# Kernel optimization log

Measured on AMD Instinct MI355X. Metric: run time of the kernel, lower is better.

The kernel has to match this reference:

```python
import jax, jax.numpy as jnp
import numpy as np

N_Q = 9      # qubits -> state dim 512
N_L = 10     # circuit layers
DIM = 2 ** N_Q
B = 16384    # batch
N_CLS = 10


def _apply_1q(psi, U, q):
    # psi: [B, 2,...,2] (N_Q qubit axes); U: [2,2] complex
    psi = jnp.moveaxis(psi, q + 1, 1)
    shp = psi.shape
    psi = jnp.einsum('ij,bjk->bik', U, psi.reshape(shp[0], 2, -1)).reshape(shp)
    return jnp.moveaxis(psi, 1, q + 1)


def _apply_2q(psi, U, q0, q1):
    # U: [4,4] complex acting on (q0, q1)
    psi = jnp.moveaxis(psi, (q0 + 1, q1 + 1), (1, 2))
    shp = psi.shape
    psi = jnp.einsum('ij,bjk->bik', U, psi.reshape(shp[0], 4, -1)).reshape(shp)
    return jnp.moveaxis(psi, (1, 2), (q0 + 1, q1 + 1))


def _rot_mat(phi, theta, omega):
    # PennyLane Rot = RZ(omega) RY(theta) RZ(phi)
    c, s = jnp.cos(theta / 2), jnp.sin(theta / 2)
    a, b = (phi + omega) / 2, (phi - omega) / 2
    return jnp.stack([
        jnp.stack([jnp.exp(-1j * a) * c, -jnp.exp(1j * b) * s]),
        jnp.stack([jnp.exp(-1j * b) * s, jnp.exp(1j * a) * c]),
    ]).astype(jnp.complex64)


def _crx_mat(t):
    c, s = jnp.cos(t / 2), jnp.sin(t / 2)
    rx = jnp.stack([jnp.stack([c + 0j, -1j * s]),
                    jnp.stack([-1j * s, c + 0j])]).astype(jnp.complex64)
    return jnp.eye(4, dtype=jnp.complex64).at[2:, 2:].set(rx)


def _layer(psi, rot_n, crx_n):
    for i in range(N_Q):
        psi = _apply_1q(psi, _rot_mat(rot_n[i, 0], rot_n[i, 1], rot_n[i, 2]), i)
    for i in range(N_Q):
        psi = _apply_2q(psi, _crx_mat(crx_n[i, 0]), i, (i + 1) % N_Q)
    return psi


def _circuit(x, rot, crx):
    # AmplitudeEmbedding(normalize=True)
    psi = (x / jnp.linalg.norm(x, axis=1, keepdims=True)).astype(jnp.complex64)
    psi = psi.reshape((x.shape[0],) + (2,) * N_Q)
    for n in range(N_L):
        psi = _layer(psi, rot[n], crx[n])
    probs = psi.real ** 2 + psi.imag ** 2
    # <Z_q> = P(bit_q = 0) - P(bit_q = 1)
    zs = []
    for q in range(N_Q):
        axes = tuple(a for a in range(1, N_Q + 1) if a != q + 1)
        p = probs.sum(axis=axes)  # [B, 2]
        zs.append(p[:, 0] - p[:, 1])
    return jnp.stack(zs, axis=1)  # [B, N_Q]


def setup_inputs() -> dict:
    key = jax.random.key(0)
    k0, k1, k2, k3, k4 = jax.random.split(key, 5)
    x = jax.random.normal(k0, (B, DIM), jnp.float32)
    rot = jax.random.normal(k1, (N_L, N_Q, 3), jnp.float32)
    crx = jax.random.normal(k2, (N_L, N_Q, 1), jnp.float32)
    fc_w = jax.random.normal(k3, (N_CLS, N_Q), jnp.float32) * 0.3
    fc_b = jax.random.normal(k4, (N_CLS,), jnp.float32) * 0.1
    return {"x": x, "rot": rot, "crx": crx, "fc_w": fc_w, "fc_b": fc_b}


def reference(x, rot, crx, fc_w, fc_b):
    z = _circuit(x, rot, crx)          # [B, 9]
    logits = z @ fc_w.T + fc_b         # [B, 10]
    return jax.nn.log_softmax(logits, axis=1)
```

## Files before the change

kernel.cpp:

```cpp
#include <hip/hip_runtime.h>
#include <hip/hip_bf16.h>
#include <math.h>

#define NQ 9
#define NL 10
#define DIM 512
#define NCLS 10
#define B_TOT 16384

#define A_OFF   ((size_t)0)
#define BT_OFF  ((size_t)16 << 20)
#define ZP_OFF  ((size_t)32 << 20)
#define WS_NEED (((size_t)96) << 20)

__device__ __forceinline__ float shx(float v, int m) { return __shfl_xor(v, m, 64); }

__device__ __forceinline__ int looks_bf16(const void* p, int count) {
  const unsigned short* u = (const unsigned short*)p;
  int n = count < 64 ? count : 64;
  int good = 0;
  for (int i = 0; i < n; ++i) {
    unsigned short v = u[i];
    int e = (v >> 7) & 0xFF;
    good += (e >= 100 && e <= 140) || ((v & 0x7FFF) == 0);
  }
  return good * 8 >= n * 7;
}

__device__ __forceinline__ float ld(const void* p, int i, int isbf) {
  if (isbf) return __uint_as_float(((unsigned)((const unsigned short*)p)[i]) << 16);
  return ((const float*)p)[i];
}

template<int M>
__device__ __forceinline__ void rot_x(float (&sr)[8], float (&si)[8], const float* u) {
  float4 uA = *(const float4*)u;
  float4 uB = *(const float4*)(u + 4);
  bool hi = (threadIdx.x & M) != 0;
  float ar = hi ? uB.z : uA.x, ai = hi ? uB.w : uA.y;
  float br = hi ? uB.x : uA.z, bi = hi ? uB.y : uA.w;
#pragma unroll
  for (int r = 0; r < 8; ++r) {
    float pr = shx(sr[r], M), pi = shx(si[r], M);
    float nr = ar * sr[r] - ai * si[r] + br * pr - bi * pi;
    float ni = ar * si[r] + ai * sr[r] + br * pi + bi * pr;
    sr[r] = nr; si[r] = ni;
  }
}
template<int S>
__device__ __forceinline__ void rot_r(float (&sr)[8], float (&si)[8], const float* u) {
  float4 uA = *(const float4*)u;
  float4 uB = *(const float4*)(u + 4);
#pragma unroll
  for (int r0 = 0; r0 < 8; ++r0) {
    if (r0 & S) continue;
    int r1 = r0 + S;
    float a0r = sr[r0], a0i = si[r0], a1r = sr[r1], a1i = si[r1];
    sr[r0] = uA.x * a0r - uA.y * a0i + uA.z * a1r - uA.w * a1i;
    si[r0] = uA.x * a0i + uA.y * a0r + uA.z * a1i + uA.w * a1r;
    sr[r1] = uB.x * a0r - uB.y * a0i + uB.z * a1r - uB.w * a1i;
    si[r1] = uB.x * a0i + uB.y * a0r + uB.z * a1i + uB.w * a1r;
  }
}
template<int MC, int MT>
__device__ __forceinline__ void crx_ll(float (&sr)[8], float (&si)[8], const float* cs) {
  bool ctrl = (threadIdx.x & MC) != 0;
  float c = ctrl ? cs[0] : 1.0f;
  float s = ctrl ? cs[1] : 0.0f;
#pragma unroll
  for (int r = 0; r < 8; ++r) {
    float pr = shx(sr[r], MT), pi = shx(si[r], MT);
    float nr = c * sr[r] + s * pi;
    float ni = c * si[r] - s * pr;
    sr[r] = nr; si[r] = ni;
  }
}
template<int MC, int ST>
__device__ __forceinline__ void crx_lr(float (&sr)[8], float (&si)[8], const float* cs) {
  bool ctrl = (threadIdx.x & MC) != 0;
  float c = ctrl ? cs[0] : 1.0f;
  float s = ctrl ? cs[1] : 0.0f;
#pragma unroll
  for (int r0 = 0; r0 < 8; ++r0) {
    if (r0 & ST) continue;
    int r1 = r0 + ST;
    float a0r = sr[r0], a0i = si[r0], a1r = sr[r1], a1i = si[r1];
    sr[r0] = c * a0r + s * a1i;  si[r0] = c * a0i - s * a1r;
    sr[r1] = c * a1r + s * a0i;  si[r1] = c * a1i - s * a0r;
  }
}
template<int PC, int ST>
__device__ __forceinline__ void crx_rr(float (&sr)[8], float (&si)[8], const float* cs) {
  float c = cs[0], s = cs[1];
#pragma unroll
  for (int r0 = 0; r0 < 8; ++r0) {
    if (r0 & ST) continue;
    if (!((r0 >> PC) & 1)) continue;
    int r1 = r0 + ST;
    float a0r = sr[r0], a0i = si[r0], a1r = sr[r1], a1i = si[r1];
    sr[r0] = c * a0r + s * a1i;  si[r0] = c * a0i - s * a1r;
    sr[r1] = c * a1r + s * a0i;  si[r1] = c * a1i - s * a0r;
  }
}
template<int PC, int MT>
__device__ __forceinline__ void crx_rl(float (&sr)[8], float (&si)[8], const float* cs) {
  float c = cs[0], s = cs[1];
#pragma unroll
  for (int r = 0; r < 8; ++r) {
    if (!((r >> PC) & 1)) continue;
    float pr = shx(sr[r], MT), pi = shx(si[r], MT);
    float nr = c * sr[r] + s * pi;
    float ni = c * si[r] - s * pr;
    sr[r] = nr; si[r] = ni;
  }
}

__device__ __forceinline__ void build_gates(const void* rot, const void* crx,
                                            float* gU, float* gCS) {
  int tid = threadIdx.x;
  __shared__ int gflags[2];
  if (tid == 0) {
    gflags[0] = looks_bf16(rot, NL * NQ * 3);
    gflags[1] = looks_bf16(crx, NL * NQ);
  }
  __syncthreads();
  if (tid < NL * NQ) {
    int frot = gflags[0], fcrx = gflags[1];
    float phi = ld(rot, tid * 3 + 0, frot);
    float th  = ld(rot, tid * 3 + 1, frot);
    float om  = ld(rot, tid * 3 + 2, frot);
    float c = cosf(0.5f * th), s = sinf(0.5f * th);
    float a = 0.5f * (phi + om), b = 0.5f * (phi - om);
    float ca = cosf(a), sa = sinf(a), cb = cosf(b), sb = sinf(b);
    float* u = gU + tid * 8;
    u[0] =  ca * c; u[1] = -sa * c;
    u[2] = -cb * s; u[3] = -sb * s;
    u[4] =  cb * s; u[5] = -sb * s;
    u[6] =  ca * c; u[7] =  sa * c;
    float t2 = 0.5f * ld(crx, tid, fcrx);
    gCS[tid * 2 + 0] = cosf(t2);
    gCS[tid * 2 + 1] = sinf(t2);
  }
  __syncthreads();
}

__device__ __forceinline__ void run_circuit(float (&sr)[8], float (&si)[8],
                                            const float* gU, const float* gCS) {
#pragma unroll 1
  for (int n = 0; n < NL; ++n) {
    const float* U  = gU  + n * NQ * 8;
    const float* CS = gCS + n * NQ * 2;
    rot_x<32>(sr, si, U + 0 * 8);
    rot_x<16>(sr, si, U + 1 * 8);
    rot_x< 8>(sr, si, U + 2 * 8);
    rot_x< 4>(sr, si, U + 3 * 8);
    rot_x< 2>(sr, si, U + 4 * 8);
    rot_x< 1>(sr, si, U + 5 * 8);
    rot_r< 4>(sr, si, U + 6 * 8);
    rot_r< 2>(sr, si, U + 7 * 8);
    rot_r< 1>(sr, si, U + 8 * 8);
    crx_ll<32, 16>(sr, si, CS + 0 * 2);
    crx_ll<16,  8>(sr, si, CS + 1 * 2);
    crx_ll< 8,  4>(sr, si, CS + 2 * 2);
    crx_ll< 4,  2>(sr, si, CS + 3 * 2);
    crx_ll< 2,  1>(sr, si, CS + 4 * 2);
    crx_lr< 1,  4>(sr, si, CS + 5 * 2);
    crx_rr< 2,  2>(sr, si, CS + 6 * 2);
    crx_rr< 1,  1>(sr, si, CS + 7 * 2);
    crx_rl< 0, 32>(sr, si, CS + 8 * 2);
  }
}

template<int M>
__device__ __forceinline__ void rot_lane2(float (&sr)[2], float (&si)[2], const float* u) {
  float4 uA = *(const float4*)u;
  float4 uB = *(const float4*)(u + 4);
  bool hi = (threadIdx.x & M) != 0;
  float ar = hi ? uB.z : uA.x, ai = hi ? uB.w : uA.y;
  float br = hi ? uB.x : uA.z, bi = hi ? uB.y : uA.w;
#pragma unroll
  for (int r = 0; r < 2; ++r) {
    float pr = shx(sr[r], M), pi = shx(si[r], M);
    float nr = ar * sr[r] - ai * si[r] + br * pr - bi * pi;
    float ni = ar * si[r] + ai * sr[r] + br * pi + bi * pr;
    sr[r] = nr; si[r] = ni;
  }
}
__device__ __forceinline__ void rot_reg2(float (&sr)[2], float (&si)[2], const float* u) {
  float4 uA = *(const float4*)u;
  float4 uB = *(const float4*)(u + 4);
  float a0r = sr[0], a0i = si[0], a1r = sr[1], a1i = si[1];
  sr[0] = uA.x * a0r - uA.y * a0i + uA.z * a1r - uA.w * a1i;
  si[0] = uA.x * a0i + uA.y * a0r + uA.z * a1i + uA.w * a1r;
  sr[1] = uB.x * a0r - uB.y * a0i + uB.z * a1r - uB.w * a1i;
  si[1] = uB.x * a0i + uB.y * a0r + uB.z * a1i + uB.w * a1r;
}
__device__ __forceinline__ void crx_lane2(float (&sr)[2], float (&si)[2],
                                          float c, float s, int MT) {
#pragma unroll
  for (int r = 0; r < 2; ++r) {
    float pr = shx(sr[r], MT), pi = shx(si[r], MT);
    float nr = c * sr[r] + s * pi;
    float ni = c * si[r] - s * pr;
    sr[r] = nr; si[r] = ni;
  }
}
__device__ __forceinline__ void crx_reg2(float (&sr)[2], float (&si)[2], float c, float s) {
  float a0r = sr[0], a0i = si[0], a1r = sr[1], a1i = si[1];
  sr[0] = c * a0r + s * a1i;  si[0] = c * a0i - s * a1r;
  sr[1] = c * a1r + s * a0i;  si[1] = c * a1i - s * a0r;
}

__global__ __launch_bounds__(256) void prep_kernel(const void* __restrict__ x,
                                                   const void* __restrict__ rot,
                                                   const void* __restrict__ crx,
                                                   __hip_bfloat16* __restrict__ A,
                                                   __hip_bfloat16* __restrict__ BT) {
  int tid = threadIdx.x;
  if (blockIdx.x < DIM) {
    __shared__ __align__(16) float gU[NL * NQ * 8];
    __shared__ __align__(16) float gCS[NL * NQ * 2];
    __shared__ float sRe[DIM], sIm[DIM];
    build_gates(rot, crx, gU, gCS);
    int lane = tid & 63, wv = tid >> 6;
    int idx0 = wv * 128 + lane * 2;
    int k = blockIdx.x;
    float sr[2], si[2];
    sr[0] = (idx0 == k) ? 1.f : 0.f;
    sr[1] = (idx0 + 1 == k) ? 1.f : 0.f;
    si[0] = si[1] = 0.f;
#pragma unroll 1
    for (int n = 0; n < NL; ++n) {
      const float* U   = gU  + n * NQ * 8;
      const float* CS  = gCS + n * NQ * 2;
      const float* CSp = gCS + (n - 1) * NQ * 2;
      __syncthreads();
      sRe[idx0] = sr[0]; sIm[idx0] = si[0];
      sRe[idx0 + 1] = sr[1]; sIm[idx0 + 1] = si[1];
      __syncthreads();
      {
        const float* U0 = U; const float* U1 = U + 8;
        int a = wv >> 1, b = wv & 1;
        float mr[4], mi[4];
#pragma unroll
        for (int w2 = 0; w2 < 4; ++w2) {
          int a2 = w2 >> 1, b2 = w2 & 1;
          float u0r = U0[(a * 2 + a2) * 2], u0i = U0[(a * 2 + a2) * 2 + 1];
          float u1r = U1[(b * 2 + b2) * 2], u1i = U1[(b * 2 + b2) * 2 + 1];
          mr[w2] = u0r * u1r - u0i * u1i;
          mi[w2] = u0r * u1i + u0i * u1r;
        }
        float x0r[4], x0i[4], v1r[4], v1i[4];
#pragma unroll
        for (int w2 = 0; w2 < 4; ++w2) {
          x0r[w2] = sRe[w2 * 128 + lane * 2 + 0];
          x0i[w2] = sIm[w2 * 128 + lane * 2 + 0];
          v1r[w2] = sRe[w2 * 128 + lane * 2 + 1];
          v1i[w2] = sIm[w2 * 128 + lane * 2 + 1];
        }
        float x1r[4], x1i[4];
        if (n > 0) {
          float cp = CSp[16], sp = CSp[17];
#pragma unroll
          for (int w2 = 0; w2 < 4; ++w2) {
            x1r[w2] = cp * v1r[w2] + sp * v1i[w2 ^ 2];
            x1i[w2] = cp * v1i[w2] - sp * v1r[w2 ^ 2];
          }
        } else {
#pragma unroll
          for (int w2 = 0; w2 < 4; ++w2) { x1r[w2] = v1r[w2]; x1i[w2] = v1i[w2]; }
        }
        float nr0 = 0.f, ni0 = 0.f, nr1 = 0.f, ni1 = 0.f;
#pragma unroll
        for (int w2 = 0; w2 < 4; ++w2) {
          nr0 += mr[w2] * x0r[w2] - mi[w2] * x0i[w2];
          ni0 += mr[w2] * x0i[w2] + mi[w2] * x0r[w2];
          nr1 += mr[w2] * x1r[w2] - mi[w2] * x1i[w2];
          ni1 += mr[w2] * x1i[w2] + mi[w2] * x1r[w2];
        }
        sr[0] = nr0; si[0] = ni0; sr[1] = nr1; si[1] = ni1;
      }
      rot_lane2<32>(sr, si, U + 2 * 8);
      rot_lane2<16>(sr, si, U + 3 * 8);
      rot_lane2< 8>(sr, si, U + 4 * 8);
      rot_lane2< 4>(sr, si, U + 5 * 8);
      rot_lane2< 2>(sr, si, U + 6 * 8);
      rot_lane2< 1>(sr, si, U + 7 * 8);
      rot_reg2(sr, si, U + 8 * 8);
      __syncthreads();
      sRe[idx0] = sr[0]; sIm[idx0] = si[0];
      sRe[idx0 + 1] = sr[1]; sIm[idx0 + 1] = si[1];
      __syncthreads();
      {
        float c = (wv & 2) ? CS[0] : 1.f, s = (wv & 2) ? CS[1] : 0.f;
        int p0 = (wv ^ 1) * 128 + lane * 2;
#pragma unroll
        for (int r = 0; r < 2; ++r) {
          float pr = sRe[p0 + r], pi = sIm[p0 + r];
          float nr = c * sr[r] + s * pi;
          float ni = c * si[r] - s * pr;
          sr[r] = nr; si[r] = ni;
        }
      }
      { float c = (wv & 1) ? CS[2] : 1.f, s = (wv & 1) ? CS[3] : 0.f;
        crx_lane2(sr, si, c, s, 32); }
      { bool ct = (lane & 32); crx_lane2(sr, si, ct ? CS[4] : 1.f, ct ? CS[5] : 0.f, 16); }
      { bool ct = (lane & 16); crx_lane2(sr, si, ct ? CS[6] : 1.f, ct ? CS[7] : 0.f, 8); }
      { bool ct = (lane &  8); crx_lane2(sr, si, ct ? CS[8] : 1.f, ct ? CS[9] : 0.f, 4); }
      { bool ct = (lane &  4); crx_lane2(sr, si, ct ? CS[10] : 1.f, ct ? CS[11] : 0.f, 2); }
      { bool ct = (lane &  2); crx_lane2(sr, si, ct ? CS[12] : 1.f, ct ? CS[13] : 0.f, 1); }
      { bool ct = (lane & 1); crx_reg2(sr, si, ct ? CS[14] : 1.f, ct ? CS[15] : 0.f); }
    }
    __syncthreads();
    sRe[idx0] = sr[0]; sIm[idx0] = si[0];
    sRe[idx0 + 1] = sr[1]; sIm[idx0 + 1] = si[1];
    __syncthreads();
    {
      const float* CS9 = gCS + (NL - 1) * NQ * 2;
      float c = CS9[16], s = CS9[17];
      int p1 = (wv ^ 2) * 128 + lane * 2 + 1;
      float pr = sRe[p1], pi = sIm[p1];
      float nr = c * sr[1] + s * pi;
      float ni = c * si[1] - s * pr;
      sr[1] = nr; si[1] = ni;
    }
#pragma unroll
    for (int r = 0; r < 2; ++r) {
      int j = idx0 + r;
      BT[(size_t)j * DIM + k]         = __float2bfloat16(sr[r]);
      BT[(size_t)(DIM + j) * DIM + k] = __float2bfloat16(si[r]);
    }
  } else {
    __shared__ int fx;
    if (tid == 0) fx = looks_bf16(x, B_TOT * DIM);
    __syncthreads();
    size_t i0 = ((size_t)(blockIdx.x - DIM) * 256 + tid) * 8;
    if (fx) {
      *(uint4*)(A + i0) = *(const uint4*)((const unsigned short*)x + i0);
    } else {
      const float4* src = (const float4*)((const float*)x + i0);
      float4 a = src[0], b = src[1];
      __hip_bfloat16 o[8];
      o[0] = __float2bfloat16(a.x); o[1] = __float2bfloat16(a.y);
      o[2] = __float2bfloat16(a.z); o[3] = __float2bfloat16(a.w);
      o[4] = __float2bfloat16(b.x); o[5] = __float2bfloat16(b.y);
      o[6] = __float2bfloat16(b.z); o[7] = __float2bfloat16(b.w);
      *(uint4*)(A + i0) = *(uint4*)o;
    }
  }
}

using frag8 = __attribute__((ext_vector_type(8))) short;
using frag4 = __attribute__((ext_vector_type(4))) float;

typedef __attribute__((address_space(1))) const unsigned int GU32;
typedef __attribute__((address_space(3))) unsigned int LU32;
__device__ __forceinline__ void async16(const void* g, void* l) {
  __builtin_amdgcn_global_load_lds((GU32*)g, (LU32*)l, 16, 0, 0);
}

#define PPITCH 136
#define PANEL (128 * 32)

__global__ __launch_bounds__(256) void gemm_z_kernel(const unsigned short* __restrict__ A,
                                                     const unsigned short* __restrict__ BT,
                                                     float* __restrict__ Zp) {
  __shared__ __align__(16) unsigned short lsm[128 * PPITCH + 16 * PPITCH];
  unsigned short* lA0 = lsm;
  unsigned short* lA1 = lsm + PANEL;
  unsigned short* lB0 = lsm + 2 * PANEL;
  unsigned short* lB1 = lsm + 3 * PANEL;
  unsigned short* pA  = lsm;
  unsigned short* STm = lsm + 128 * PPITCH;
  int bid = blockIdx.x;
  int xcd = bid & 7;
  int slot = bid >> 3;
  int n0 = (slot & 7) * 128;
  int m0 = (xcd * 16 + (slot >> 3)) * 128;
  int tid = threadIdx.x;
  int wv = tid >> 6, lane = tid & 63;
  int wm = wv >> 1, wn = wv & 1;
  int row = lane & 15, quad = lane >> 4;
  for (int i = tid; i < 16 * 128; i += 256) {
    int q = i >> 7, k2 = i & 127;
    int j = (n0 + k2) & 511;
    float sg = (q < 9) ? (((j >> (8 - q)) & 1) ? -1.f : 1.f) : (q == 9 ? 1.f : 0.f);
    __hip_bfloat16 h = __float2bfloat16(sg);
    STm[q * PPITCH + k2] = *(unsigned short*)&h;
  }
  int srow = wv * 32 + (lane >> 2);
  int scol = (lane & 3) * 8;
  const unsigned short* gA = A + (size_t)(m0 + srow) * 512 + scol;
  const unsigned short* gB = BT + (size_t)(n0 + srow) * 512 + scol;
  frag4 acc[4][4] = {};
#pragma unroll 1
  for (int k0 = 0; k0 < 512; k0 += 64) {
    __syncthreads();
    async16(gA + k0,                 &lA0[(wv * 32) * 32]);
    async16(gA + k0 + 16 * 512,      &lA0[(wv * 32 + 16) * 32]);
    async16(gA + k0 + 32,            &lA1[(wv * 32) * 32]);
    async16(gA + k0 + 32 + 16 * 512, &lA1[(wv * 32 + 16) * 32]);
    async16(gB + k0,                 &lB0[(wv * 32) * 32]);
    async16(gB + k0 + 16 * 512,      &lB0[(wv * 32 + 16) * 32]);
    async16(gB + k0 + 32,            &lB1[(wv * 32) * 32]);
    async16(gB + k0 + 32 + 16 * 512, &lB1[(wv * 32 + 16) * 32]);
    __syncthreads();
    {
      frag8 af[4], bf[4];
#pragma unroll
      for (int i = 0; i < 4; ++i) {
        af[i] = *(const frag8*)(&lA0[(wm * 64 + i * 16 + row) * 32 + quad * 8]);
        bf[i] = *(const frag8*)(&lB0[(wn * 64 + i * 16 + row) * 32 + quad * 8]);
      }
#pragma unroll
      for (int mi = 0; mi < 4; ++mi)
#pragma unroll
        for (int ni = 0; ni < 4; ++ni)
          acc[mi][ni] = __builtin_amdgcn_mfma_f32_16x16x32_bf16(af[mi], bf[ni],
                                                                acc[mi][ni], 0, 0, 0);
    }
    {
      frag8 af[4], bf[4];
#pragma unroll
      for (int i = 0; i < 4; ++i) {
        af[i] = *(const frag8*)(&lA1[(wm * 64 + i * 16 + row) * 32 + quad * 8]);
        bf[i] = *(const frag8*)(&lB1[(wn * 64 + i * 16 + row) * 32 + quad * 8]);
      }
#pragma unroll
      for (int mi = 0; mi < 4; ++mi)
#pragma unroll
        for (int ni = 0; ni < 4; ++ni)
          acc[mi][ni] = __builtin_amdgcn_mfma_f32_16x16x32_bf16(af[mi], bf[ni],
                                                                acc[mi][ni], 0, 0, 0);
    }
  }
  __syncthreads();
#pragma unroll
  for (int mi = 0; mi < 4; ++mi)
#pragma unroll
    for (int ni = 0; ni < 4; ++ni)
#pragma unroll
      for (int rg = 0; rg < 4; ++rg) {
        float v = acc[mi][ni][rg];
        float p = v * v;
        int mrow = wm * 64 + mi * 16 + quad * 4 + rg;
        int k2 = wn * 64 + ni * 16 + row;
        __hip_bfloat16 h = __float2bfloat16(p);
        pA[mrow * PPITCH + k2] = *(unsigned short*)&h;
      }
  __syncthreads();
  frag8 b2[4];
#pragma unroll
  for (int kk = 0; kk < 4; ++kk)
    b2[kk] = *(const frag8*)(&STm[row * PPITCH + kk * 32 + quad * 8]);
  frag4 zacc2[2] = {};
#pragma unroll
  for (int t = 0; t < 2; ++t) {
    int mt = wv + t * 4;
#pragma unroll
    for (int kk = 0; kk < 4; ++kk) {
      frag8 a2 = *(const frag8*)(&pA[(mt * 16 + row) * PPITCH + kk * 32 + quad * 8]);
      zacc2[t] = __builtin_amdgcn_mfma_f32_16x16x32_bf16(a2, b2[kk], zacc2[t], 0, 0, 0);
    }
  }
  int panel = n0 >> 7;
  if (row < 10) {
#pragma unroll
    for (int t = 0; t < 2; ++t) {
      int mt = wv + t * 4;
#pragma unroll
      for (int rg = 0; rg < 4; ++rg) {
        int mrow = m0 + mt * 16 + quad * 4 + rg;
        Zp[(size_t)panel * (B_TOT * 10) + (size_t)mrow * 10 + row] = zacc2[t][rg];
      }
    }
  }
}

__global__ __launch_bounds__(256) void zred_kernel(const float* __restrict__ Zp,
                                                   const void* __restrict__ fcw,
                                                   const void* __restrict__ fcb,
                                                   float* __restrict__ out) {
  __shared__ int flags[2];
  __shared__ float sW[NCLS * NQ];
  __shared__ float sB[NCLS];
  int tid = threadIdx.x;
  if (tid == 0) {
    flags[0] = looks_bf16(fcw, NCLS * NQ);
    flags[1] = looks_bf16(fcb, NCLS);
  }
  __syncthreads();
  if (tid < NCLS * NQ) sW[tid] = ld(fcw, tid, flags[0]);
  if (tid < NCLS)      sB[tid] = ld(fcb, tid, flags[1]);
  __syncthreads();
  int row = blockIdx.x * 256 + tid;
  float z[10];
#pragma unroll
  for (int q = 0; q < 10; ++q) z[q] = 0.f;
#pragma unroll
  for (int pnl = 0; pnl < 8; ++pnl) {
    const float* p = Zp + (size_t)pnl * (B_TOT * 10) + (size_t)row * 10;
#pragma unroll
    for (int q = 0; q < 10; ++q) z[q] += p[q];
  }
  float invP = 1.0f / z[9];
#pragma unroll
  for (int q = 0; q < NQ; ++q) z[q] *= invP;
  float lg[NCLS], mx = -1e30f;
#pragma unroll
  for (int k = 0; k < NCLS; ++k) {
    float t = sB[k];
#pragma unroll
    for (int q = 0; q < NQ; ++q) t += z[q] * sW[k * NQ + q];
    lg[k] = t; mx = fmaxf(mx, t);
  }
  float se = 0.f;
#pragma unroll
  for (int k = 0; k < NCLS; ++k) se += expf(lg[k] - mx);
  float lse = mx + logf(se);
#pragma unroll
  for (int k = 0; k < NCLS; ++k) out[(size_t)row * NCLS + k] = lg[k] - lse;
}

__global__ __launch_bounds__(256) void qnn_kernel(
    const void* __restrict__ x, const void* __restrict__ rot,
    const void* __restrict__ crx, const void* __restrict__ fcw,
    const void* __restrict__ fcb, float* __restrict__ out) {
  __shared__ __align__(16) float gU[NL * NQ * 8];
  __shared__ __align__(16) float gCS[NL * NQ * 2];
  __shared__ int flags[3];
  int tid = threadIdx.x;
  if (tid == 0) {
    flags[0] = looks_bf16(x, B_TOT * DIM);
    flags[1] = looks_bf16(fcw, NCLS * NQ);
    flags[2] = looks_bf16(fcb, NCLS);
  }
  build_gates(rot, crx, gU, gCS);
  __syncthreads();
  int wid = (blockIdx.x * blockDim.x + tid) >> 6;
  int lane = tid & 63;
  float sr[8], si[8];
  if (flags[0]) {
    const uint4 u = *(const uint4*)((const unsigned short*)x + (size_t)wid * DIM + lane * 8);
    sr[0] = __uint_as_float(u.x << 16); sr[1] = __uint_as_float(u.x & 0xffff0000u);
    sr[2] = __uint_as_float(u.y << 16); sr[3] = __uint_as_float(u.y & 0xffff0000u);
    sr[4] = __uint_as_float(u.z << 16); sr[5] = __uint_as_float(u.z & 0xffff0000u);
    sr[6] = __uint_as_float(u.w << 16); sr[7] = __uint_as_float(u.w & 0xffff0000u);
  } else {
    const float4* xf = (const float4*)((const float*)x + (size_t)wid * DIM) + lane * 2;
    float4 a = xf[0], b = xf[1];
    sr[0] = a.x; sr[1] = a.y; sr[2] = a.z; sr[3] = a.w;
    sr[4] = b.x; sr[5] = b.y; sr[6] = b.z; sr[7] = b.w;
  }
  float nrm = 0.f;
#pragma unroll
  for (int r = 0; r < 8; ++r) { nrm += sr[r] * sr[r]; si[r] = 0.f; }
#pragma unroll
  for (int m = 1; m < 64; m <<= 1) nrm += shx(nrm, m);
  float inv = rsqrtf(nrm);
  inv = inv * (1.5f - 0.5f * nrm * inv * inv);
#pragma unroll
  for (int r = 0; r < 8; ++r) sr[r] *= inv;
  run_circuit(sr, si, gU, gCS);
  float p[8], P = 0.f;
#pragma unroll
  for (int r = 0; r < 8; ++r) { p[r] = sr[r] * sr[r] + si[r] * si[r]; P += p[r]; }
  float z[NQ];
#pragma unroll
  for (int q = 0; q < 6; ++q) z[q] = (lane & (32 >> q)) ? -P : P;
  z[6] = z[7] = z[8] = 0.f;
#pragma unroll
  for (int r = 0; r < 8; ++r) {
    z[6] += (r & 4) ? -p[r] : p[r];
    z[7] += (r & 2) ? -p[r] : p[r];
    z[8] += (r & 1) ? -p[r] : p[r];
  }
#pragma unroll
  for (int m = 1; m < 64; m <<= 1) {
#pragma unroll
    for (int q = 0; q < NQ; ++q) z[q] += shx(z[q], m);
  }
  int ffw = flags[1], ffb = flags[2];
  float lg[NCLS], mx = -1e30f;
#pragma unroll
  for (int k = 0; k < NCLS; ++k) {
    float t = ld(fcb, k, ffb);
#pragma unroll
    for (int q = 0; q < NQ; ++q) t += z[q] * ld(fcw, k * NQ + q, ffw);
    lg[k] = t; mx = fmaxf(mx, t);
  }
  float se = 0.f;
#pragma unroll
  for (int k = 0; k < NCLS; ++k) se += expf(lg[k] - mx);
  float lse = mx + logf(se);
  if (lane < NCLS) out[(size_t)wid * NCLS + lane] = lg[lane] - lse;
}

extern "C" void kernel_launch(void* const* d_in, const int* in_sizes, int n_in,
                              void* d_out, int out_size, void* d_ws, size_t ws_size,
                              hipStream_t stream) {
  const void* x   = d_in[0];
  const void* rot = d_in[1];
  const void* crx = d_in[2];
  const void* fcw = d_in[3];
  const void* fcb = d_in[4];
  float* out = (float*)d_out;
  if (ws_size >= WS_NEED) {
    __hip_bfloat16* A  = (__hip_bfloat16*)((char*)d_ws + A_OFF);
    __hip_bfloat16* BT = (__hip_bfloat16*)((char*)d_ws + BT_OFF);
    float*          Zp = (float*)((char*)d_ws + ZP_OFF);
    prep_kernel<<<DIM + (B_TOT * DIM) / (256 * 8), 256, 0, stream>>>(x, rot, crx, A, BT);
    gemm_z_kernel<<<(B_TOT / 128) * (1024 / 128), 256, 0, stream>>>(
        (const unsigned short*)A, (const unsigned short*)BT, Zp);
    zred_kernel<<<B_TOT / 256, 256, 0, stream>>>(Zp, fcw, fcb, out);
  } else {
    qnn_kernel<<<(B_TOT * 64) / 256, 256, 0, stream>>>(x, rot, crx, fcw, fcb, out);
  }
}
```

Before: 143.2 us.

## Rewrite GEMM as 256x256 tiles with double-buffered async loads and swizzled LDS

```diff
diff --git a/kernel.cpp b/kernel.cpp
--- a/kernel.cpp
+++ b/kernel.cpp
@@ -359,125 +359,155 @@
   __builtin_amdgcn_global_load_lds((GU32*)g, (LU32*)l, 16, 0, 0);
 }
 
-#define PPITCH 136
-#define PANEL (128 * 32)
-
-__global__ __launch_bounds__(256) void gemm_z_kernel(const unsigned short* __restrict__ A,
-                                                     const unsigned short* __restrict__ BT,
-                                                     float* __restrict__ Zp) {
-  __shared__ __align__(16) unsigned short lsm[128 * PPITCH + 16 * PPITCH];
-  unsigned short* lA0 = lsm;
-  unsigned short* lA1 = lsm + PANEL;
-  unsigned short* lB0 = lsm + 2 * PANEL;
-  unsigned short* lB1 = lsm + 3 * PANEL;
-  unsigned short* pA  = lsm;
-  unsigned short* STm = lsm + 128 * PPITCH;
+#define VM(N) asm volatile("s_waitcnt vmcnt(" #N ")" ::: "memory")
+#define BARR  do { __builtin_amdgcn_sched_barrier(0); \
+                   __builtin_amdgcn_s_barrier(); \
+                   __builtin_amdgcn_sched_barrier(0); } while (0)
+
+#define STG_A(NB, T1, H) do { \
+  async16(gA + ((size_t)((H) * 128) * 512 + (T1) * 64),     dA + (NB) * 16384 + (H) * 8192); \
+  async16(gA + ((size_t)((H) * 128 + 8) * 512 + (T1) * 64), dA + (NB) * 16384 + (H) * 8192 + 512); \
+} while (0)
+#define STG_B(NB, T1, H) do { \
+  async16(gB + ((size_t)((H) * 128) * 512 + (T1) * 64),     dB + (NB) * 16384 + (H) * 8192); \
+  async16(gB + ((size_t)((H) * 128 + 8) * 512 + (T1) * 64), dB + (NB) * 16384 + (H) * 8192 + 512); \
+} while (0)
+
+#define PHASE(CURB, QM, QN, STG, VMC) do { \
+  frag8 paf[4][2], pbf[2][2]; \
+  _Pragma("unroll") \
+  for (int mi = 0; mi < 4; ++mi) { \
+    _Pragma("unroll") \
+    for (int kk = 0; kk < 2; ++kk) \
+      paf[mi][kk] = *(const frag8*)(lsm + (CURB) * 16384 + \
+        ((QM) * 128 + wm * 64 + mi * 16 + r15) * 64 + \
+        (((kk * 4 + quad) ^ (r15 & 7)) * 8)); \
+  } \
+  _Pragma("unroll") \
+  for (int ni = 0; ni < 2; ++ni) { \
+    _Pragma("unroll") \
+    for (int kk = 0; kk < 2; ++kk) \
+      pbf[ni][kk] = *(const frag8*)(lsm + 32768 + (CURB) * 16384 + \
+        ((QN) * 128 + wn * 32 + ni * 16 + r15) * 64 + \
+        (((kk * 4 + quad) ^ (r15 & 7)) * 8)); \
+  } \
+  STG; \
+  __builtin_amdgcn_s_setprio(1); \
+  _Pragma("unroll") \
+  for (int mi = 0; mi < 4; ++mi) { \
+    _Pragma("unroll") \
+    for (int ni = 0; ni < 2; ++ni) { \
+      acc[QM][mi][QN][ni] = __builtin_amdgcn_mfma_f32_16x16x32_bf16( \
+          paf[mi][0], pbf[ni][0], acc[QM][mi][QN][ni], 0, 0, 0); \
+      acc[QM][mi][QN][ni] = __builtin_amdgcn_mfma_f32_16x16x32_bf16( \
+          paf[mi][1], pbf[ni][1], acc[QM][mi][QN][ni], 0, 0, 0); \
+    } \
+  } \
+  __builtin_amdgcn_s_setprio(0); \
+  VMC; \
+} while (0)
+
+__global__ __launch_bounds__(512, 2) void gemm_z_kernel(const unsigned short* __restrict__ A,
+                                                        const unsigned short* __restrict__ BT,
+                                                        float* __restrict__ Zp) {
+  __shared__ __align__(16) unsigned short lsm[65536];
   int bid = blockIdx.x;
   int xcd = bid & 7;
-  int slot = bid >> 3;
-  int n0 = (slot & 7) * 128;
-  int m0 = (xcd * 16 + (slot >> 3)) * 128;
+  int ii = bid >> 3;
+  int m0 = (xcd * 8 + (ii >> 2)) * 256;
+  int n0 = (ii & 3) * 256;
   int tid = threadIdx.x;
   int wv = tid >> 6, lane = tid & 63;
-  int wm = wv >> 1, wn = wv & 1;
-  int row = lane & 15, quad = lane >> 4;
-  for (int i = tid; i < 16 * 128; i += 256) {
-    int q = i >> 7, k2 = i & 127;
-    int j = (n0 + k2) & 511;
-    float sg = (q < 9) ? (((j >> (8 - q)) & 1) ? -1.f : 1.f) : (q == 9 ? 1.f : 0.f);
-    __hip_bfloat16 h = __float2bfloat16(sg);
-    STm[q * PPITCH + k2] = *(unsigned short*)&h;
-  }
-  int srow = wv * 32 + (lane >> 2);
-  int scol = (lane & 3) * 8;
-  const unsigned short* gA = A + (size_t)(m0 + srow) * 512 + scol;
-  const unsigned short* gB = BT + (size_t)(n0 + srow) * 512 + scol;
-  frag4 acc[4][4] = {};
+  int wm = wv >> 2, wn = wv & 3;
+  int r15 = lane & 15, quad = lane >> 4;
+  int lr3 = lane >> 3;
+  int scol = ((lane & 7) ^ lr3) * 8;
+  const unsigned short* gA = A + (size_t)(m0 + wv * 16 + lr3) * 512 + scol;
+  const unsigned short* gB = BT + (size_t)(n0 + wv * 16 + lr3) * 512 + scol;
+  unsigned short* dA = lsm + wv * 16 * 64;
+  unsigned short* dB = lsm + 32768 + wv * 16 * 64;
+
+  frag4 acc[2][4][2][2] = {};
+
+  STG_A(0, 0, 0); STG_B(0, 0, 0); STG_A(0, 0, 1); STG_B(0, 0, 1);
+  VM(4);
+  BARR;
+
 #pragma unroll 1
-  for (int k0 = 0; k0 < 512; k0 += 64) {
-    __syncthreads();
-    async16(gA + k0,                 &lA0[(wv * 32) * 32]);
-    async16(gA + k0 + 16 * 512,      &lA0[(wv * 32 + 16) * 32]);
-    async16(gA + k0 + 32,            &lA1[(wv * 32) * 32]);
-    async16(gA + k0 + 32 + 16 * 512, &lA1[(wv * 32 + 16) * 32]);
-    async16(gB + k0,                 &lB0[(wv * 32) * 32]);
-    async16(gB + k0 + 16 * 512,      &lB0[(wv * 32 + 16) * 32]);
-    async16(gB + k0 + 32,            &lB1[(wv * 32) * 32]);
-    async16(gB + k0 + 32 + 16 * 512, &lB1[(wv * 32 + 16) * 32]);
-    __syncthreads();
-    {
-      frag8 af[4], bf[4];
-#pragma unroll
-      for (int i = 0; i < 4; ++i) {
-        af[i] = *(const frag8*)(&lA0[(wm * 64 + i * 16 + row) * 32 + quad * 8]);
-        bf[i] = *(const frag8*)(&lB0[(wn * 64 + i * 16 + row) * 32 + quad * 8]);
-      }
-#pragma unroll
-      for (int mi = 0; mi < 4; ++mi)
-#pragma unroll
-        for (int ni = 0; ni < 4; ++ni)
-          acc[mi][ni] = __builtin_amdgcn_mfma_f32_16x16x32_bf16(af[mi], bf[ni],
-                                                                acc[mi][ni], 0, 0, 0);
+  for (int t = 0; t < 7; ++t) {
+    const int cur = t & 1, nb = cur ^ 1;
+    PHASE(cur, 0, 0, STG_A(nb, t + 1, 0), VM(4)); BARR;
+    PHASE(cur, 1, 0, STG_B(nb, t + 1, 0), VM(4)); BARR;
+    PHASE(cur, 0, 1, STG_A(nb, t + 1, 1), ;);
+    PHASE(cur, 1, 1, STG_B(nb, t + 1, 1), VM(4)); BARR;
+  }
+  PHASE(1, 0, 0, ;, VM(2)); BARR;
+  PHASE(1, 1, 0, ;, VM(0)); BARR;
+  PHASE(1, 0, 1, ;, ;);
+  PHASE(1, 1, 1, ;, ;);
+  __syncthreads();
+
+#pragma unroll
+  for (int qm = 0; qm < 2; ++qm)
+#pragma unroll
+    for (int mi = 0; mi < 4; ++mi)
+#pragma unroll
+      for (int qn = 0; qn < 2; ++qn)
+#pragma unroll
+        for (int ni = 0; ni < 2; ++ni)
+#pragma unroll
+          for (int rg = 0; rg < 4; ++rg) {
+            float v = acc[qm][mi][qn][ni][rg];
+            float p = v * v;
+            int prow = qm * 128 + wm * 64 + mi * 16 + quad * 4 + rg;
+            int pcol = qn * 128 + wn * 32 + ni * 16 + r15;
+            int phys = (pcol >> 3) ^ (prow & 7);
+            __hip_bfloat16 h = __float2bfloat16(p);
+            lsm[prow * 256 + phys * 8 + (pcol & 7)] = *(unsigned short*)&h;
+          }
+  __syncthreads();
+
+  frag8 b2[8];
+#pragma unroll
+  for (int kk = 0; kk < 8; ++kk) {
+    union { frag8 f; unsigned short u[8]; } bb;
+#pragma unroll
+    for (int e = 0; e < 8; ++e) {
+      int j = (n0 + kk * 32 + quad * 8 + e) & 511;
+      unsigned short us;
+      if (r15 < 9)      us = ((((unsigned)j) >> ((8 - r15) & 31)) & 1) ? 0xBF80 : 0x3F80;
+      else if (r15 == 9) us = 0x3F80;
+      else               us = 0;
+      bb.u[e] = us;
     }
-    {
-      frag8 af[4], bf[4];
-#pragma unroll
-      for (int i = 0; i < 4; ++i) {
-        af[i] = *(const frag8*)(&lA1[(wm * 64 + i * 16 + row) * 32 + quad * 8]);
-        bf[i] = *(const frag8*)(&lB1[(wn * 64 + i * 16 + row) * 32 + quad * 8]);
-      }
-#pragma unroll
-      for (int mi = 0; mi < 4; ++mi)
-#pragma unroll
-        for (int ni = 0; ni < 4; ++ni)
-          acc[mi][ni] = __builtin_amdgcn_mfma_f32_16x16x32_bf16(af[mi], bf[ni],
-                                                                acc[mi][ni], 0, 0, 0);
+    b2[kk] = bb.f;
+  }
+  frag4 z2[2] = {};
+#pragma unroll
+  for (int tt = 0; tt < 2; ++tt) {
+    int mt = wv + tt * 8;
+#pragma unroll
+    for (int kk = 0; kk < 8; ++kk) {
+      frag8 a2 = *(const frag8*)(lsm + (mt * 16 + r15) * 256 +
+                                 (((kk * 4 + quad) ^ (r15 & 7)) * 8));
+      z2[tt] = __builtin_amdgcn_mfma_f32_16x16x32_bf16(a2, b2[kk], z2[tt], 0, 0, 0);
     }
   }
-  __syncthreads();
-#pragma unroll
-  for (int mi = 0; mi < 4; ++mi)
-#pragma unroll
-    for (int ni = 0; ni < 4; ++ni)
-#pragma unroll
-      for (int rg = 0; rg < 4; ++rg) {
-        float v = acc[mi][ni][rg];
-        float p = v * v;
-        int mrow = wm * 64 + mi * 16 + quad * 4 + rg;
-        int k2 = wn * 64 + ni * 16 + row;
-        __hip_bfloat16 h = __float2bfloat16(p);
-        pA[mrow * PPITCH + k2] = *(unsigned short*)&h;
-      }
-  __syncthreads();
-  frag8 b2[4];
-#pragma unroll
-  for (int kk = 0; kk < 4; ++kk)
-    b2[kk] = *(const frag8*)(&STm[row * PPITCH + kk * 32 + quad * 8]);
-  frag4 zacc2[2] = {};
-#pragma unroll
-  for (int t = 0; t < 2; ++t) {
-    int mt = wv + t * 4;
-#pragma unroll
-    for (int kk = 0; kk < 4; ++kk) {
-      frag8 a2 = *(const frag8*)(&pA[(mt * 16 + row) * PPITCH + kk * 32 + quad * 8]);
-      zacc2[t] = __builtin_amdgcn_mfma_f32_16x16x32_bf16(a2, b2[kk], zacc2[t], 0, 0, 0);
-    }
-  }
-  int panel = n0 >> 7;
-  if (row < 10) {
-#pragma unroll
-    for (int t = 0; t < 2; ++t) {
-      int mt = wv + t * 4;
+  int panel = n0 >> 8;
+  if (r15 < 10) {
+#pragma unroll
+    for (int tt = 0; tt < 2; ++tt) {
+      int mt = wv + tt * 8;
 #pragma unroll
       for (int rg = 0; rg < 4; ++rg) {
         int mrow = m0 + mt * 16 + quad * 4 + rg;
-        Zp[(size_t)panel * (B_TOT * 10) + (size_t)mrow * 10 + row] = zacc2[t][rg];
+        Zp[(size_t)panel * (B_TOT * 10) + (size_t)mrow * 10 + r15] = z2[tt][rg];
       }
     }
   }
 }
 
-__global__ __launch_bounds__(256) void zred_kernel(const float* __restrict__ Zp,
+__global__ __launch_bounds__(128) void zred_kernel(const float* __restrict__ Zp,
                                                    const void* __restrict__ fcw,
                                                    const void* __restrict__ fcb,
                                                    float* __restrict__ out) {
@@ -493,12 +523,12 @@
   if (tid < NCLS * NQ) sW[tid] = ld(fcw, tid, flags[0]);
   if (tid < NCLS)      sB[tid] = ld(fcb, tid, flags[1]);
   __syncthreads();
-  int row = blockIdx.x * 256 + tid;
+  int row = blockIdx.x * 128 + tid;
   float z[10];
 #pragma unroll
   for (int q = 0; q < 10; ++q) z[q] = 0.f;
 #pragma unroll
-  for (int pnl = 0; pnl < 8; ++pnl) {
+  for (int pnl = 0; pnl < 4; ++pnl) {
     const float* p = Zp + (size_t)pnl * (B_TOT * 10) + (size_t)row * 10;
 #pragma unroll
     for (int q = 0; q < 10; ++q) z[q] += p[q];
@@ -610,9 +640,9 @@
     __hip_bfloat16* BT = (__hip_bfloat16*)((char*)d_ws + BT_OFF);
     float*          Zp = (float*)((char*)d_ws + ZP_OFF);
     prep_kernel<<<DIM + (B_TOT * DIM) / (256 * 8), 256, 0, stream>>>(x, rot, crx, A, BT);
-    gemm_z_kernel<<<(B_TOT / 128) * (1024 / 128), 256, 0, stream>>>(
+    gemm_z_kernel<<<(B_TOT / 256) * (1024 / 256), 512, 0, stream>>>(
         (const unsigned short*)A, (const unsigned short*)BT, Zp);
-    zred_kernel<<<B_TOT / 256, 256, 0, stream>>>(Zp, fcw, fcb, out);
+    zred_kernel<<<B_TOT / 128, 128, 0, stream>>>(Zp, fcw, fcb, out);
   } else {
     qnn_kernel<<<(B_TOT * 64) / 256, 256, 0, stream>>>(x, rot, crx, fcw, fcb, out);
   }
```

After: 135.8 us. 1.05x faster.
